# Kernel tuning notes

Hardware: AMD Instinct MI355X
Metric: run time of the kernel (lower is better)

Reference implementation:

```python
import jax, jax.numpy as jnp
import numpy as np

B, C, H, W = 4, 256, 64, 64
CH = C // 2


def setup_inputs() -> dict:
    key = jax.random.key(0)
    ks = jax.random.split(key, 8)
    s_in = 1.0 / np.sqrt(C)  # conv2d default init scale (fan_in = C for 1x1)
    return {
        "a": jax.random.normal(ks[0], (B, C, H, W), dtype=jnp.float32),
        "p": jax.random.normal(ks[1], (B, C, H, W), dtype=jnp.float32),
        "Wq": jax.random.uniform(ks[2], (CH, C), jnp.float32, -s_in, s_in),
        "bq": jax.random.uniform(ks[3], (CH,), jnp.float32, -s_in, s_in),
        "Wk": jax.random.uniform(ks[4], (CH, C), jnp.float32, -s_in, s_in),
        "bk": jax.random.uniform(ks[5], (CH,), jnp.float32, -s_in, s_in),
        "Wv": jax.random.uniform(ks[6], (C, C), jnp.float32, -s_in, s_in),
        "bv": jax.random.uniform(ks[7], (C,), jnp.float32, -s_in, s_in),
    }


def reference(a, p, Wq, bq, Wk, bk, Wv, bv):
    b, c, h, w = a.shape
    hw = h * w
    # 1x1 convs == per-pixel channel matmuls; flatten spatial dims to hw
    Q = jnp.einsum('oc,bchw->bohw', Wq, a).reshape(b, -1, hw) + bq[None, :, None]   # [B, C/2, HW]
    K = jnp.einsum('oc,bchw->bohw', Wk, p).reshape(b, -1, hw) + bk[None, :, None]   # [B, C/2, HW]
    V = jnp.einsum('oc,bchw->bohw', Wv, p).reshape(b, -1, hw) + bv[None, :, None]   # [B, C,   HW]
    # attn[b,m,n] = softmax_n( Q[:, :, m] . K[:, :, n] )
    attn = jax.nn.softmax(jnp.einsum('bcm,bcn->bmn', Q, K), axis=-1)                # [B, HW, HW]
    # out[b,c,m] = sum_n V[b,c,n] * attn[b,m,n]  (V @ attn^T)
    out = jnp.einsum('bcn,bmn->bcm', V, attn).reshape(b, c, h, w)
    return out + a
```

## Files before the change

kernel.cpp:

```cpp
#include <hip/hip_runtime.h>
#include <stdint.h>

#define B_ 4
#define C_ 256
#define CH_ 128
#define HW_ 4096
#define L2E 1.44269504f
#define SHIFT_L2 14.4269504f

typedef __bf16 bf16;
typedef __bf16 v8bf __attribute__((ext_vector_type(8)));
typedef __bf16 v4bf __attribute__((ext_vector_type(4)));
typedef float v4f __attribute__((ext_vector_type(4)));
struct f4 { float x, y, z, w; };

#define GAS __attribute__((address_space(1)))
#define LAS __attribute__((address_space(3)))

__device__ __forceinline__ void async_copy16(const void* gptr, void* lptr) {
  __builtin_amdgcn_global_load_lds((GAS void*)gptr, (LAS void*)lptr, 16, 0, 0);
}

__global__ __launch_bounds__(512)
void proj_kernel(const float* __restrict__ a, const float* __restrict__ p,
                 const float* __restrict__ Wq, const float* __restrict__ bq,
                 const float* __restrict__ Wk, const float* __restrict__ bk,
                 const float* __restrict__ Wv, const float* __restrict__ bv,
                 bf16* __restrict__ Qt, bf16* __restrict__ Kt, bf16* __restrict__ Vn)
{
  __shared__ bf16 Xt[64 * 266];
  __shared__ bf16 Ds[9600];

  const int t = threadIdx.x;
  const int lane = t & 63;
  const int w = t >> 6;
  const int l15 = lane & 15;
  const int q = lane >> 4;

  const int s0 = blockIdx.x * 64;
  const int b = blockIdx.y;
  const int z = blockIdx.z;

  const float* X    = (z == 0) ? a  : p;
  const float* W    = (z == 0) ? Wq : (z == 1 ? Wk : Wv);
  const float* bias = (z == 0) ? bq : (z == 1 ? bk : bv);
  const int nh = (z == 2) ? 2 : 1;

  const float* Xb = X + ((size_t)b * C_) * HW_;
  for (int j = 0; j < 16; ++j) {
    int linear = t + 512 * j;
    int s = linear & 63;
    int cp = linear >> 6;
    float x0 = Xb[(size_t)(2 * cp) * HW_ + s0 + s];
    float x1 = Xb[(size_t)(2 * cp + 1) * HW_ + s0 + s];
    unsigned short u0 = __builtin_bit_cast(unsigned short, (bf16)x0);
    unsigned short u1 = __builtin_bit_cast(unsigned short, (bf16)x1);
    *(unsigned int*)&Xt[s * 266 + 2 * cp] = (unsigned int)u0 | ((unsigned int)u1 << 16);
  }
  __syncthreads();

  for (int h = 0; h < nh; ++h) {
    v8bf Af[8];
    const float* Wrow = W + (size_t)(h * 128 + 16 * w + l15) * C_;
    #pragma unroll
    for (int kk = 0; kk < 8; ++kk) {
      f4 f0 = *(const f4*)&Wrow[kk * 32 + q * 8];
      f4 f1 = *(const f4*)&Wrow[kk * 32 + q * 8 + 4];
      v8bf f;
      f[0] = (bf16)f0.x; f[1] = (bf16)f0.y; f[2] = (bf16)f0.z; f[3] = (bf16)f0.w;
      f[4] = (bf16)f1.x; f[5] = (bf16)f1.y; f[6] = (bf16)f1.z; f[7] = (bf16)f1.w;
      Af[kk] = f;
    }

    v4f acc[4];
    #pragma unroll
    for (int ns = 0; ns < 4; ++ns) { v4f zz = {0.f, 0.f, 0.f, 0.f}; acc[ns] = zz; }
    #pragma unroll
    for (int ns = 0; ns < 4; ++ns)
      #pragma unroll
      for (int kk = 0; kk < 8; ++kk) {
        v8bf Bf = *(const v8bf*)&Xt[(16 * ns + l15) * 266 + kk * 32 + q * 8];
        acc[ns] = __builtin_amdgcn_mfma_f32_16x16x32_bf16(Af[kk], Bf, acc[ns], 0, 0, 0);
      }

    if (z < 2) {
      #pragma unroll
      for (int ns = 0; ns < 4; ++ns)
        #pragma unroll
        for (int r = 0; r < 4; ++r)
          Ds[(16 * ns + l15) * 150 + 16 * w + 4 * q + r] =
              (bf16)(acc[ns][r] + bias[16 * w + 4 * q + r]);
      __syncthreads();
      bf16* dst = (z == 0) ? Qt : Kt;
      #pragma unroll
      for (int i = 0; i < 2; ++i) {
        int idx = t + 512 * i;
        int s = idx >> 4, ch = (idx & 15) * 8;
        *(v8bf*)&dst[((size_t)b * HW_ + s0 + s) * CH_ + ch] = *(const v8bf*)&Ds[s * 150 + ch];
      }
    } else {
      #pragma unroll
      for (int ns = 0; ns < 4; ++ns)
        #pragma unroll
        for (int r = 0; r < 4; ++r)
          Ds[(16 * w + 4 * q + r) * 72 + l15 * 4 + ns] =
              (bf16)(acc[ns][r] + bias[h * 128 + 16 * w + 4 * q + r]);
      __syncthreads();
      #pragma unroll
      for (int i = 0; i < 2; ++i) {
        int idx = t + 512 * i;
        int o = idx >> 3, ch = (idx & 7) * 8;
        *(v8bf*)&Vn[((size_t)b * C_ + h * 128 + o) * HW_ + s0 + ch] = *(const v8bf*)&Ds[o * 72 + ch];
      }
      if (h == 0) __syncthreads();
    }
  }
}

#define LDS_V 16640
#define LDS_P 49920
#define LDS_TOTAL 68352

__global__ __launch_bounds__(256, 2)
void attn_kernel(const bf16* __restrict__ Qt, const bf16* __restrict__ Kt,
                 const bf16* __restrict__ Vn, const float* __restrict__ a,
                 float* __restrict__ out, bf16* __restrict__ Op,
                 float* __restrict__ Ls, int nsplit)
{
  extern __shared__ char smem[];
  const int t = threadIdx.x;
  const int lane = t & 63;
  const int w = t >> 6;
  const int l15 = lane & 15;
  const int q = lane >> 4;
  const int b = blockIdx.y;
  const int sp = blockIdx.z;
  const int m0 = blockIdx.x * 128;

  v8bf Qf[2][4];
  #pragma unroll
  for (int s = 0; s < 2; ++s) {
    const bf16* qrow = Qt + ((size_t)b * HW_ + m0 + 32 * w + 16 * s + l15) * CH_;
    #pragma unroll
    for (int kk = 0; kk < 4; ++kk)
      Qf[s][kk] = *(const v8bf*)&qrow[kk * 32 + q * 8];
  }

  v4f O[2][16];
  #pragma unroll
  for (int s = 0; s < 2; ++s)
    #pragma unroll
    for (int cs = 0; cs < 16; ++cs) { v4f zz = {0.f, 0.f, 0.f, 0.f}; O[s][cs] = zz; }
  float lsum[2][4];
  #pragma unroll
  for (int s = 0; s < 2; ++s)
    #pragma unroll
    for (int r = 0; r < 4; ++r) lsum[s][r] = 0.f;

  const bf16* Kb = Kt + (size_t)b * HW_ * CH_;
  const bf16* Vb = Vn + (size_t)b * C_ * HW_;
  char* Pbase = smem + LDS_P + w * 4608;

  const int NT = 64 / nsplit;
  const int t0 = sp * NT;

  auto stageK = [&](int n0) {
    #pragma unroll
    for (int j = 0; j < 4; ++j) {
      int i = 4 * j + w;
      async_copy16(Kb + ((size_t)(n0 + i + 16 * q)) * CH_ + l15 * 8, smem + i * 1040);
    }
  };
  auto stageV = [&](int n0) {
    #pragma unroll
    for (int j = 0; j < 8; ++j) {
      int i = 4 * j + w;
      async_copy16(Vb + ((size_t)(i + 32 * (lane >> 3))) * HW_ + n0 + (lane & 7) * 8,
                   smem + LDS_V + i * 1040);
    }
  };

  stageK(t0 * 64);
  stageV(t0 * 64);
  __syncthreads();

  for (int nt = 0; nt < NT; ++nt) {
    int n0 = (t0 + nt) * 64;

    v4f S[2][4];
    #pragma unroll
    for (int s = 0; s < 2; ++s)
      #pragma unroll
      for (int sub = 0; sub < 4; ++sub) { v4f zz = {0.f, 0.f, 0.f, 0.f}; S[s][sub] = zz; }
    #pragma unroll
    for (int sub = 0; sub < 4; ++sub)
      #pragma unroll
      for (int kk = 0; kk < 4; ++kk) {
        v8bf Kf = *(const v8bf*)(smem + l15 * 1040 + sub * 256 + kk * 64 + q * 16);
        S[0][sub] = __builtin_amdgcn_mfma_f32_16x16x32_bf16(Qf[0][kk], Kf, S[0][sub], 0, 0, 0);
        S[1][sub] = __builtin_amdgcn_mfma_f32_16x16x32_bf16(Qf[1][kk], Kf, S[1][sub], 0, 0, 0);
      }

    __syncthreads();
    if (nt + 1 < NT) stageK(n0 + 64);

    #pragma unroll
    for (int s = 0; s < 2; ++s)
      #pragma unroll
      for (int r = 0; r < 4; ++r) {
        v4bf pp;
        float p0 = exp2f(S[s][0][r] * L2E - SHIFT_L2);
        float p1 = exp2f(S[s][1][r] * L2E - SHIFT_L2);
        float p2 = exp2f(S[s][2][r] * L2E - SHIFT_L2);
        float p3 = exp2f(S[s][3][r] * L2E - SHIFT_L2);
        pp[0] = (bf16)p0; pp[1] = (bf16)p1; pp[2] = (bf16)p2; pp[3] = (bf16)p3;
        lsum[s][r] += (p0 + p1) + (p2 + p3);
        *(v4bf*)(Pbase + (16 * s + 4 * q + r) * 144 + l15 * 8) = pp;
      }

    v8bf Pf[2][2];
    #pragma unroll
    for (int s = 0; s < 2; ++s)
      #pragma unroll
      for (int kk = 0; kk < 2; ++kk)
        Pf[s][kk] = *(const v8bf*)(Pbase + (16 * s + l15) * 144 + kk * 64 + q * 16);

    #pragma unroll
    for (int cs = 0; cs < 16; ++cs)
      #pragma unroll
      for (int kk = 0; kk < 2; ++kk) {
        v8bf Vf = *(const v8bf*)(smem + LDS_V +
                                 (16 * (cs & 1) + l15) * 1040 + (cs >> 1) * 128 + kk * 64 + q * 16);
        O[0][cs] = __builtin_amdgcn_mfma_f32_16x16x32_bf16(Pf[0][kk], Vf, O[0][cs], 0, 0, 0);
        O[1][cs] = __builtin_amdgcn_mfma_f32_16x16x32_bf16(Pf[1][kk], Vf, O[1][cs], 0, 0, 0);
      }

    __syncthreads();
    if (nt + 1 < NT) stageV(n0 + 64);
  }

  float lfin[2][4];
  #pragma unroll
  for (int s = 0; s < 2; ++s)
    #pragma unroll
    for (int r = 0; r < 4; ++r) {
      float l = lsum[s][r];
      l += __shfl_xor(l, 1);
      l += __shfl_xor(l, 2);
      l += __shfl_xor(l, 4);
      l += __shfl_xor(l, 8);
      lfin[s][r] = l;
    }

  if (nsplit > 1 && l15 == 0) {
    #pragma unroll
    for (int s = 0; s < 2; ++s)
      #pragma unroll
      for (int r = 0; r < 4; ++r) {
        int m = m0 + 32 * w + 16 * s + 4 * q + r;
        Ls[((size_t)sp * B_ + b) * HW_ + m] = lfin[s][r];
      }
  }

  bf16* T = (bf16*)smem;
  float linv[2][4];
  #pragma unroll
  for (int s = 0; s < 2; ++s)
    #pragma unroll
    for (int r = 0; r < 4; ++r) linv[s][r] = (nsplit == 1) ? 1.0f / lfin[s][r] : 1.0f;

  for (int round = 0; round < 2; ++round) {
    __syncthreads();
    if ((w >> 1) == round) {
      bf16* Tw = T + (w & 1) * 12288;
      #pragma unroll
      for (int s = 0; s < 2; ++s)
        #pragma unroll
        for (int cs = 0; cs < 16; ++cs)
          #pragma unroll
          for (int r = 0; r < 4; ++r)
            Tw[(16 * cs + l15) * 48 + 16 * s + 4 * q + r] = (bf16)(O[s][cs][r] * linv[s][r]);
    }
    __syncthreads();
    #pragma unroll
    for (int it = 0; it < 8; ++it) {
      int idx = t + 256 * it;
      int tt = idx >> 10;
      int c = (idx >> 2) & 255;
      int mc = idx & 3;
      int wavew = round * 2 + tt;
      int mg = m0 + 32 * wavew + mc * 8;
      v8bf val = *(const v8bf*)&T[tt * 12288 + c * 48 + mc * 8];
      if (nsplit == 1) {
        size_t gi = ((size_t)b * C_ + c) * HW_ + mg;
        #pragma unroll
        for (int j2 = 0; j2 < 8; ++j2) out[gi + j2] = (float)val[j2] + a[gi + j2];
      } else {
        size_t gi = (((size_t)sp * B_ + b) * C_ + c) * HW_ + mg;
        *(v8bf*)&Op[gi] = val;
      }
    }
  }
}

__global__ __launch_bounds__(256)
void combine_kernel(const bf16* __restrict__ Op, const float* __restrict__ Ls,
                    const float* __restrict__ a, float* __restrict__ out, int nsplit)
{
  int idx = blockIdx.x * 256 + threadIdx.x;
  int m8 = (idx & (HW_ / 8 - 1)) * 8;
  int bc = idx >> 9;
  int b = bc >> 8;

  float acc[8], L[8];
  #pragma unroll
  for (int j = 0; j < 8; ++j) { acc[j] = 0.f; L[j] = 0.f; }
  for (int s = 0; s < nsplit; ++s) {
    v8bf o = *(const v8bf*)&Op[((size_t)s * B_ * C_ + bc) * HW_ + m8];
    const float* lp = Ls + ((size_t)s * B_ + b) * HW_ + m8;
    #pragma unroll
    for (int j = 0; j < 8; ++j) { acc[j] += (float)o[j]; L[j] += lp[j]; }
  }
  const float* ap = a + (size_t)bc * HW_ + m8;
  float* op = out + (size_t)bc * HW_ + m8;
  #pragma unroll
  for (int j = 0; j < 8; ++j) op[j] = acc[j] / L[j] + ap[j];
}

extern "C" void kernel_launch(void* const* d_in, const int* in_sizes, int n_in,
                              void* d_out, int out_size, void* d_ws, size_t ws_size,
                              hipStream_t stream) {
  const float* a  = (const float*)d_in[0];
  const float* p  = (const float*)d_in[1];
  const float* Wq = (const float*)d_in[2];
  const float* bq = (const float*)d_in[3];
  const float* Wk = (const float*)d_in[4];
  const float* bk = (const float*)d_in[5];
  const float* Wv = (const float*)d_in[6];
  const float* bv = (const float*)d_in[7];
  float* out = (float*)d_out;

  bf16* Qt = (bf16*)d_ws;
  bf16* Kt = Qt + (size_t)B_ * HW_ * CH_;
  bf16* Vn = Kt + (size_t)B_ * HW_ * CH_;

  const size_t proj_bytes = 16777216ull;
  const size_t part_bytes = (size_t)B_ * C_ * HW_ * 2;
  const size_t stat_bytes = (size_t)B_ * HW_ * 4;
  auto need = [&](int S) { return proj_bytes + (size_t)S * (part_bytes + stat_bytes); };

  int S;
  if      (ws_size >= need(4)) S = 4;
  else if (ws_size >= need(2)) S = 2;
  else                         S = 1;

  bf16* Op = (bf16*)((char*)d_ws + proj_bytes);
  float* Ls = (float*)((char*)d_ws + proj_bytes + (size_t)S * part_bytes);

  dim3 pg(HW_ / 64, B_, 3);
  proj_kernel<<<pg, 512, 0, stream>>>(a, p, Wq, bq, Wk, bk, Wv, bv, Qt, Kt, Vn);

  hipFuncSetAttribute(reinterpret_cast<const void*>(&attn_kernel),
                      hipFuncAttributeMaxDynamicSharedMemorySize, LDS_TOTAL);
  dim3 ag(HW_ / 128, B_, S);
  attn_kernel<<<ag, 256, LDS_TOTAL, stream>>>(Qt, Kt, Vn, a, out, Op, Ls, S);

  if (S > 1) {
    int nblk = (B_ * C_ * HW_ / 8) / 256;
    combine_kernel<<<nblk, 256, 0, stream>>>(Op, Ls, a, out, S);
  }
}
```

Before: 186.2 us.

## Compute transposed scores to keep P in registers, raise occupancy and split

The attention kernel now computes S^T (K as the A operand), so each lane's exponentiated scores already form the bf16 B-fragment layout for the PV MFMA. This removes the P round-trip through LDS, cuts LDS to allow 3 blocks per CU, and reduces row-sum reductions to two cross-quad shuffles. The projection kernel splits the V projection into two z-slices for more parallel blocks and permutes the V store layout to match the new P column ordering. The split count can rise to 8 when workspace allows, which adds combine traffic.

```diff
diff --git a/kernel.cpp b/kernel.cpp
--- a/kernel.cpp
+++ b/kernel.cpp
@@ -10,7 +10,6 @@
 
 typedef __bf16 bf16;
 typedef __bf16 v8bf __attribute__((ext_vector_type(8)));
-typedef __bf16 v4bf __attribute__((ext_vector_type(4)));
 typedef float v4f __attribute__((ext_vector_type(4)));
 struct f4 { float x, y, z, w; };
 
@@ -41,10 +40,11 @@
   const int b = blockIdx.y;
   const int z = blockIdx.z;
 
-  const float* X    = (z == 0) ? a  : p;
-  const float* W    = (z == 0) ? Wq : (z == 1 ? Wk : Wv);
-  const float* bias = (z == 0) ? bq : (z == 1 ? bk : bv);
-  const int nh = (z == 2) ? 2 : 1;
+  const float* X = (z == 0) ? a : p;
+  const float* W; const float* bias;
+  if (z == 0)      { W = Wq; bias = bq; }
+  else if (z == 1) { W = Wk; bias = bk; }
+  else             { W = Wv + (size_t)(z - 2) * 128 * C_; bias = bv + (z - 2) * 128; }
 
   const float* Xb = X + ((size_t)b * C_) * HW_;
   for (int j = 0; j < 16; ++j) {
@@ -57,71 +57,71 @@
     unsigned short u1 = __builtin_bit_cast(unsigned short, (bf16)x1);
     *(unsigned int*)&Xt[s * 266 + 2 * cp] = (unsigned int)u0 | ((unsigned int)u1 << 16);
   }
+
+  v8bf Af[8];
+  const float* Wrow = W + (size_t)(16 * w + l15) * C_;
+  #pragma unroll
+  for (int kk = 0; kk < 8; ++kk) {
+    f4 f0 = *(const f4*)&Wrow[kk * 32 + q * 8];
+    f4 f1 = *(const f4*)&Wrow[kk * 32 + q * 8 + 4];
+    v8bf f;
+    f[0] = (bf16)f0.x; f[1] = (bf16)f0.y; f[2] = (bf16)f0.z; f[3] = (bf16)f0.w;
+    f[4] = (bf16)f1.x; f[5] = (bf16)f1.y; f[6] = (bf16)f1.z; f[7] = (bf16)f1.w;
+    Af[kk] = f;
+  }
+
   __syncthreads();
 
-  for (int h = 0; h < nh; ++h) {
-    v8bf Af[8];
-    const float* Wrow = W + (size_t)(h * 128 + 16 * w + l15) * C_;
+  v4f acc[4];
+  #pragma unroll
+  for (int ns = 0; ns < 4; ++ns) { v4f zz = {0.f, 0.f, 0.f, 0.f}; acc[ns] = zz; }
+  #pragma unroll
+  for (int ns = 0; ns < 4; ++ns)
     #pragma unroll
     for (int kk = 0; kk < 8; ++kk) {
-      f4 f0 = *(const f4*)&Wrow[kk * 32 + q * 8];
-      f4 f1 = *(const f4*)&Wrow[kk * 32 + q * 8 + 4];
-      v8bf f;
-      f[0] = (bf16)f0.x; f[1] = (bf16)f0.y; f[2] = (bf16)f0.z; f[3] = (bf16)f0.w;
-      f[4] = (bf16)f1.x; f[5] = (bf16)f1.y; f[6] = (bf16)f1.z; f[7] = (bf16)f1.w;
-      Af[kk] = f;
-    }
-
-    v4f acc[4];
-    #pragma unroll
-    for (int ns = 0; ns < 4; ++ns) { v4f zz = {0.f, 0.f, 0.f, 0.f}; acc[ns] = zz; }
+      v8bf Bf = *(const v8bf*)&Xt[(16 * ns + l15) * 266 + kk * 32 + q * 8];
+      acc[ns] = __builtin_amdgcn_mfma_f32_16x16x32_bf16(Af[kk], Bf, acc[ns], 0, 0, 0);
+    }
+
+  if (z < 2) {
     #pragma unroll
     for (int ns = 0; ns < 4; ++ns)
       #pragma unroll
-      for (int kk = 0; kk < 8; ++kk) {
-        v8bf Bf = *(const v8bf*)&Xt[(16 * ns + l15) * 266 + kk * 32 + q * 8];
-        acc[ns] = __builtin_amdgcn_mfma_f32_16x16x32_bf16(Af[kk], Bf, acc[ns], 0, 0, 0);
+      for (int r = 0; r < 4; ++r)
+        Ds[(16 * ns + l15) * 150 + 16 * w + 4 * q + r] =
+            (bf16)(acc[ns][r] + bias[16 * w + 4 * q + r]);
+    __syncthreads();
+    bf16* dst = (z == 0) ? Qt : Kt;
+    #pragma unroll
+    for (int i = 0; i < 2; ++i) {
+      int idx = t + 512 * i;
+      int s = idx >> 4, ch = (idx & 15) * 8;
+      *(v8bf*)&dst[((size_t)b * HW_ + s0 + s) * CH_ + ch] = *(const v8bf*)&Ds[s * 150 + ch];
+    }
+  } else {
+    int o0 = (z - 2) * 128;
+    #pragma unroll
+    for (int ns = 0; ns < 4; ++ns)
+      #pragma unroll
+      for (int r = 0; r < 4; ++r) {
+        int pos = 32 * (ns >> 1) + 8 * (l15 >> 2) + 4 * (ns & 1) + (l15 & 3);
+        Ds[(16 * w + 4 * q + r) * 72 + pos] =
+            (bf16)(acc[ns][r] + bias[16 * w + 4 * q + r]);
       }
-
-    if (z < 2) {
-      #pragma unroll
-      for (int ns = 0; ns < 4; ++ns)
-        #pragma unroll
-        for (int r = 0; r < 4; ++r)
-          Ds[(16 * ns + l15) * 150 + 16 * w + 4 * q + r] =
-              (bf16)(acc[ns][r] + bias[16 * w + 4 * q + r]);
-      __syncthreads();
-      bf16* dst = (z == 0) ? Qt : Kt;
-      #pragma unroll
-      for (int i = 0; i < 2; ++i) {
-        int idx = t + 512 * i;
-        int s = idx >> 4, ch = (idx & 15) * 8;
-        *(v8bf*)&dst[((size_t)b * HW_ + s0 + s) * CH_ + ch] = *(const v8bf*)&Ds[s * 150 + ch];
-      }
-    } else {
-      #pragma unroll
-      for (int ns = 0; ns < 4; ++ns)
-        #pragma unroll
-        for (int r = 0; r < 4; ++r)
-          Ds[(16 * w + 4 * q + r) * 72 + l15 * 4 + ns] =
-              (bf16)(acc[ns][r] + bias[h * 128 + 16 * w + 4 * q + r]);
-      __syncthreads();
-      #pragma unroll
-      for (int i = 0; i < 2; ++i) {
-        int idx = t + 512 * i;
-        int o = idx >> 3, ch = (idx & 7) * 8;
-        *(v8bf*)&Vn[((size_t)b * C_ + h * 128 + o) * HW_ + s0 + ch] = *(const v8bf*)&Ds[o * 72 + ch];
-      }
-      if (h == 0) __syncthreads();
+    __syncthreads();
+    #pragma unroll
+    for (int i = 0; i < 2; ++i) {
+      int idx = t + 512 * i;
+      int o = idx >> 3, ch = (idx & 7) * 8;
+      *(v8bf*)&Vn[((size_t)b * C_ + o0 + o) * HW_ + s0 + ch] = *(const v8bf*)&Ds[o * 72 + ch];
     }
   }
 }
 
 #define LDS_V 16640
-#define LDS_P 49920
-#define LDS_TOTAL 68352
-
-__global__ __launch_bounds__(256, 2)
+#define LDS_TOTAL 49920
+
+__global__ __launch_bounds__(256, 3)
 void attn_kernel(const bf16* __restrict__ Qt, const bf16* __restrict__ Kt,
                  const bf16* __restrict__ Vn, const float* __restrict__ a,
                  float* __restrict__ out, bf16* __restrict__ Op,
@@ -151,15 +151,10 @@
   for (int s = 0; s < 2; ++s)
     #pragma unroll
     for (int cs = 0; cs < 16; ++cs) { v4f zz = {0.f, 0.f, 0.f, 0.f}; O[s][cs] = zz; }
-  float lsum[2][4];
-  #pragma unroll
-  for (int s = 0; s < 2; ++s)
-    #pragma unroll
-    for (int r = 0; r < 4; ++r) lsum[s][r] = 0.f;
+  float lsum[2] = {0.f, 0.f};
 
   const bf16* Kb = Kt + (size_t)b * HW_ * CH_;
   const bf16* Vb = Vn + (size_t)b * C_ * HW_;
-  char* Pbase = smem + LDS_P + w * 4608;
 
   const int NT = 64 / nsplit;
   const int t0 = sp * NT;
@@ -187,43 +182,39 @@
   for (int nt = 0; nt < NT; ++nt) {
     int n0 = (t0 + nt) * 64;
 
-    v4f S[2][4];
-    #pragma unroll
-    for (int s = 0; s < 2; ++s)
-      #pragma unroll
-      for (int sub = 0; sub < 4; ++sub) { v4f zz = {0.f, 0.f, 0.f, 0.f}; S[s][sub] = zz; }
+    v4f St[4][2];
+    #pragma unroll
+    for (int sub = 0; sub < 4; ++sub)
+      #pragma unroll
+      for (int s = 0; s < 2; ++s) { v4f zz = {0.f, 0.f, 0.f, 0.f}; St[sub][s] = zz; }
     #pragma unroll
     for (int sub = 0; sub < 4; ++sub)
       #pragma unroll
       for (int kk = 0; kk < 4; ++kk) {
         v8bf Kf = *(const v8bf*)(smem + l15 * 1040 + sub * 256 + kk * 64 + q * 16);
-        S[0][sub] = __builtin_amdgcn_mfma_f32_16x16x32_bf16(Qf[0][kk], Kf, S[0][sub], 0, 0, 0);
-        S[1][sub] = __builtin_amdgcn_mfma_f32_16x16x32_bf16(Qf[1][kk], Kf, S[1][sub], 0, 0, 0);
+        St[sub][0] = __builtin_amdgcn_mfma_f32_16x16x32_bf16(Kf, Qf[0][kk], St[sub][0], 0, 0, 0);
+        St[sub][1] = __builtin_amdgcn_mfma_f32_16x16x32_bf16(Kf, Qf[1][kk], St[sub][1], 0, 0, 0);
       }
 
     __syncthreads();
     if (nt + 1 < NT) stageK(n0 + 64);
 
-    #pragma unroll
-    for (int s = 0; s < 2; ++s)
-      #pragma unroll
-      for (int r = 0; r < 4; ++r) {
-        v4bf pp;
-        float p0 = exp2f(S[s][0][r] * L2E - SHIFT_L2);
-        float p1 = exp2f(S[s][1][r] * L2E - SHIFT_L2);
-        float p2 = exp2f(S[s][2][r] * L2E - SHIFT_L2);
-        float p3 = exp2f(S[s][3][r] * L2E - SHIFT_L2);
-        pp[0] = (bf16)p0; pp[1] = (bf16)p1; pp[2] = (bf16)p2; pp[3] = (bf16)p3;
-        lsum[s][r] += (p0 + p1) + (p2 + p3);
-        *(v4bf*)(Pbase + (16 * s + 4 * q + r) * 144 + l15 * 8) = pp;
-      }
-
     v8bf Pf[2][2];
     #pragma unroll
-    for (int s = 0; s < 2; ++s)
+    for (int s = 0; s < 2; ++s) {
+      float ls = 0.f;
       #pragma unroll
       for (int kk = 0; kk < 2; ++kk)
-        Pf[s][kk] = *(const v8bf*)(Pbase + (16 * s + l15) * 144 + kk * 64 + q * 16);
+        #pragma unroll
+        for (int a2 = 0; a2 < 2; ++a2)
+          #pragma unroll
+          for (int r = 0; r < 4; ++r) {
+            float pv = exp2f(St[2 * kk + a2][s][r] * L2E - SHIFT_L2);
+            Pf[s][kk][4 * a2 + r] = (bf16)pv;
+            ls += pv;
+          }
+      lsum[s] += ls;
+    }
 
     #pragma unroll
     for (int cs = 0; cs < 16; ++cs)
@@ -239,36 +230,29 @@
     if (nt + 1 < NT) stageV(n0 + 64);
   }
 
-  float lfin[2][4];
+  float lfin[2];
+  #pragma unroll
+  for (int s = 0; s < 2; ++s) {
+    float l = lsum[s];
+    l += __shfl_xor(l, 16);
+    l += __shfl_xor(l, 32);
+    lfin[s] = l;
+  }
+
+  if (nsplit > 1 && lane < 16) {
+    #pragma unroll
+    for (int s = 0; s < 2; ++s)
+      Ls[((size_t)sp * B_ + b) * HW_ + m0 + 32 * w + 16 * s + lane] = lfin[s];
+  }
+
+  float linv[2][4];
   #pragma unroll
   for (int s = 0; s < 2; ++s)
     #pragma unroll
-    for (int r = 0; r < 4; ++r) {
-      float l = lsum[s][r];
-      l += __shfl_xor(l, 1);
-      l += __shfl_xor(l, 2);
-      l += __shfl_xor(l, 4);
-      l += __shfl_xor(l, 8);
-      lfin[s][r] = l;
-    }
-
-  if (nsplit > 1 && l15 == 0) {
-    #pragma unroll
-    for (int s = 0; s < 2; ++s)
-      #pragma unroll
-      for (int r = 0; r < 4; ++r) {
-        int m = m0 + 32 * w + 16 * s + 4 * q + r;
-        Ls[((size_t)sp * B_ + b) * HW_ + m] = lfin[s][r];
-      }
-  }
+    for (int r = 0; r < 4; ++r)
+      linv[s][r] = (nsplit == 1) ? 1.0f / __shfl(lfin[s], 4 * q + r) : 1.0f;
 
   bf16* T = (bf16*)smem;
-  float linv[2][4];
-  #pragma unroll
-  for (int s = 0; s < 2; ++s)
-    #pragma unroll
-    for (int r = 0; r < 4; ++r) linv[s][r] = (nsplit == 1) ? 1.0f / lfin[s][r] : 1.0f;
-
   for (int round = 0; round < 2; ++round) {
     __syncthreads();
     if ((w >> 1) == round) {
@@ -350,18 +334,17 @@
   auto need = [&](int S) { return proj_bytes + (size_t)S * (part_bytes + stat_bytes); };
 
   int S;
-  if      (ws_size >= need(4)) S = 4;
+  if      (ws_size >= need(8)) S = 8;
+  else if (ws_size >= need(4)) S = 4;
   else if (ws_size >= need(2)) S = 2;
   else                         S = 1;
 
   bf16* Op = (bf16*)((char*)d_ws + proj_bytes);
   float* Ls = (float*)((char*)d_ws + proj_bytes + (size_t)S * part_bytes);
 
-  dim3 pg(HW_ / 64, B_, 3);
+  dim3 pg(HW_ / 64, B_, 4);
   proj_kernel<<<pg, 512, 0, stream>>>(a, p, Wq, bq, Wk, bk, Wv, bv, Qt, Kt, Vn);
 
-  hipFuncSetAttribute(reinterpret_cast<const void*>(&attn_kernel),
-                      hipFuncAttributeMaxDynamicSharedMemorySize, LDS_TOTAL);
   dim3 ag(HW_ / 128, B_, S);
   attn_kernel<<<ag, 256, LDS_TOTAL, stream>>>(Qt, Kt, Vn, a, out, Op, Ls, S);
 
```

Measured after the change: 405.3 us. 118% more time.
